# Optimization experiments

Measured on AMD Instinct MI355X. Metric: run time of the kernel, lower is better.

The kernel has to match this reference:

```python
import jax, jax.numpy as jnp
import numpy as np

N = 100000      # points
M = 12500       # cluster centers
E0 = 1600000    # point-level edges
E1 = 400000     # cluster-level edges
F_IN = 4        # raw point feature dim (e.g. intensity + extras)
D = 64          # hidden feature width
N_CLASSES = 8


def setup_inputs() -> dict:
    key = jax.random.key(0)
    ks = jax.random.split(key, 20)
    s = 0.05
    d = {}
    d["features"] = jax.random.normal(ks[0], (N, F_IN), jnp.float32)
    d["points"] = jax.random.normal(ks[1], (N, 3), jnp.float32)
    d["cluster_centers"] = jax.random.normal(ks[2], (M, 3), jnp.float32)
    d["l0_edges"] = jax.random.randint(ks[3], (E0, 2), 0, N)
    d["l1_edges"] = jax.random.randint(ks[4], (E1, 2), 0, M)
    d["labels"] = jax.random.randint(ks[5], (N,), 0, M)
    # Feature_extract MLP
    d["W_fe"] = s * jax.random.normal(ks[6], (F_IN + 3, D), jnp.float32)
    d["b_fe"] = jnp.zeros((D,), jnp.float32)
    # 4 Mini_GNN layers (layer2, layer2_1, layer6, layer6_1), stacked
    d["mini_We"] = s * jax.random.normal(ks[7], (4, D + 3, D), jnp.float32)
    d["mini_be"] = jnp.zeros((4, D), jnp.float32)
    d["mini_Wu"] = s * jax.random.normal(ks[8], (4, D, D), jnp.float32)
    d["mini_bu"] = jnp.zeros((4, D), jnp.float32)
    # Mini_to_Large
    d["W_m1"] = s * jax.random.normal(ks[9], (D + 3, D), jnp.float32)
    d["b_m1"] = jnp.zeros((D,), jnp.float32)
    d["W_m2"] = s * jax.random.normal(ks[10], (D, D), jnp.float32)
    d["b_m2"] = jnp.zeros((D,), jnp.float32)
    # 2 GNN layers on cluster graph (layer4, layer4_1), stacked
    d["gnn_We"] = s * jax.random.normal(ks[11], (2, D + 3, D), jnp.float32)
    d["gnn_be"] = jnp.zeros((2, D), jnp.float32)
    d["gnn_Wu"] = s * jax.random.normal(ks[12], (2, D, D), jnp.float32)
    d["gnn_bu"] = jnp.zeros((2, D), jnp.float32)
    # Large_to_Mini
    d["W_l"] = s * jax.random.normal(ks[13], (D + 3, D), jnp.float32)
    d["b_l"] = jnp.zeros((D,), jnp.float32)
    # Classifier
    d["W_c"] = s * jax.random.normal(ks[14], (D, N_CLASSES), jnp.float32)
    d["b_c"] = jnp.zeros((N_CLASSES,), jnp.float32)
    return d


def _gnn_layer(feat, pos, edges, We, be, Wu, bu, n_nodes):
    """PointGNN-style layer: gather -> edge MLP -> scatter max -> update MLP -> residual."""
    src, dst = edges[:, 0], edges[:, 1]
    e_in = jnp.concatenate([pos[src] - pos[dst], feat[src]], axis=-1)  # [E, 3+D]
    h = jax.nn.relu(e_in @ We + be)                                     # [E, D]
    agg = jax.ops.segment_max(h, dst, num_segments=n_nodes)            # [n, D]
    agg = jnp.where(jnp.isneginf(agg), 0.0, agg)  # nodes with no in-edges -> 0
    return jax.nn.relu(agg @ Wu + bu) + feat


def reference(features, points, cluster_centers, l0_edges, l1_edges, labels,
              W_fe, b_fe, mini_We, mini_be, mini_Wu, mini_bu,
              W_m1, b_m1, W_m2, b_m2, gnn_We, gnn_be, gnn_Wu, gnn_bu,
              W_l, b_l, W_c, b_c):
    rel = points - cluster_centers[labels]  # [N, 3] point pos relative to its cluster
    # layer1: Feature_extract
    f1 = jax.nn.relu(jnp.concatenate([features, rel], -1) @ W_fe + b_fe)
    # layer2 / layer2_1: Mini_GNN (scatter max) on point graph
    f2 = _gnn_layer(f1, points, l0_edges, mini_We[0], mini_be[0], mini_Wu[0], mini_bu[0], N)
    f2_1 = _gnn_layer(f2, points, l0_edges, mini_We[1], mini_be[1], mini_Wu[1], mini_bu[1], N)
    # layer3: Mini_to_Large (scatter sum by labels)
    h = jax.nn.relu(jnp.concatenate([f2_1, rel], -1) @ W_m1 + b_m1)
    c = jax.ops.segment_sum(h, labels, num_segments=M)  # [M, D]
    f3 = jax.nn.relu(c @ W_m2 + b_m2)
    # layer4 / layer4_1: GNN (scatter max) on cluster graph
    f4 = _gnn_layer(f3, cluster_centers, l1_edges, gnn_We[0], gnn_be[0], gnn_Wu[0], gnn_bu[0], M)
    f4_1 = _gnn_layer(f4, cluster_centers, l1_edges, gnn_We[1], gnn_be[1], gnn_Wu[1], gnn_bu[1], M)
    # layer5: Large_to_Mini (gather by labels)
    f5 = jax.nn.relu(jnp.concatenate([f4_1[labels], rel], -1) @ W_l + b_l)
    # layer6 / layer6_1 with residual skips per call()
    f6 = _gnn_layer(f5, points, l0_edges, mini_We[2], mini_be[2], mini_Wu[2], mini_bu[2], N)
    f6 = f6 + f2_1
    f6_1 = _gnn_layer(f6, points, l0_edges, mini_We[3], mini_be[3], mini_Wu[3], mini_bu[3], N)
    final = f6_1 + f2
    return final @ W_c + b_c  # [N, N_CLASSES] per-point logits
```

## Files before the change

### kernel.cpp

```cpp
#include <hip/hip_runtime.h>


#define N_PTS   100000
#define M_CL    12500
#define E0_N    1600000
#define E1_N    400000

#define NB      256
#define NCOPY   32
#define RANGE0  391
#define RANGE1  49
#define NCH0    782
#define NCH1    196
#define NCHL    49
#define CAP0    7168
#define CAP1    2048
#define CAPL    768

#define LSTR    72

typedef unsigned short ushortT;
typedef short  short8 __attribute__((ext_vector_type(8)));
typedef short  s4v    __attribute__((ext_vector_type(4)));
typedef float  v4f    __attribute__((ext_vector_type(4)));
typedef _Float16 h2   __attribute__((ext_vector_type(2)));
typedef unsigned u4v  __attribute__((ext_vector_type(4)));

__device__ inline ushortT f2bf(float x){
  union{float f; unsigned u;} v; v.f = x;
  unsigned r = v.u + 0x7fffu + ((v.u >> 16) & 1u);
  return (ushortT)(r >> 16);
}
__device__ inline float bf2f(ushortT h){
  union{unsigned u; float f;} v; v.u = ((unsigned)h) << 16;
  return v.f;
}
__device__ inline ushortT f2h(float x){
  union{_Float16 h; ushortT u;} v; v.h = (_Float16)x;
  return v.u;
}
__device__ inline float h2f(ushortT u){
  union{ushortT u; _Float16 h;} v; v.u = u;
  return (float)v.h;
}
__device__ inline h2 pkmax(h2 a, h2 b){ return __builtin_elementwise_max(a, b); }
__device__ inline h2 u2h(unsigned u){ union{unsigned u; h2 h;} v{u}; return v.h; }


struct WSrc { const float* p[22]; };

__global__ __launch_bounds__(256) void k_init_wprep(WSrc s, ushortT* __restrict__ wt, ushortT* __restrict__ wtc,
                                                    float* __restrict__ wpp,
                                                    int* b0, int* b1, int* bL){
  int blk = blockIdx.x;
  if (blk == 0){
    int t = threadIdx.x;
    #pragma unroll
    for (int k=0;k<NCOPY;++k){
      b0[k*NB + t] = 0; b1[k*NB + t] = 0; bL[k*NB + t] = 0;
    }
    return;
  }
  int slot = blk - 1;
  if (slot < 15){
    const float* src = s.p[slot];
    ushortT* dst = wt + slot*4096;
    for (int e=threadIdx.x; e<4096; e+=256){
      int nn = e>>6, p = e&63;
      int kk = (p&3)*16 + (p>>2);
      dst[e] = f2bf(src[kk*64+nn]);
    }
  } else if (slot == 15){
    const float* src = s.p[15];
    for (int e=threadIdx.x; e<1024; e+=256){
      int nn = e>>6, p = e&63;
      int kk = (p&3)*16 + (p>>2);
      wtc[e] = (nn<8) ? f2bf(src[kk*8+nn]) : (ushortT)0;
    }
  } else {
    for (int e=threadIdx.x; e<6*192; e+=256){
      int i = e/192, rem = e - i*192, r = rem>>6, p = rem&63;
      wpp[e] = s.p[16+i][r*64 + ((p&3)*16 + (p>>2))];
    }
  }
}


template<int RANGE, bool LAB>
__device__ void sort_chunk(const int* __restrict__ edges, int E, int c,
                           unsigned* __restrict__ slab, int* __restrict__ offC,
                           int* __restrict__ btot,
                           unsigned* slds, int* hist, int* pfx){
  int tid = threadIdx.x;
  int base = c*2048;
  int cnt = E - base; if (cnt > 2048) cnt = 2048;
  hist[tid] = 0;
  __syncthreads();
  int bk[8]; unsigned pk[8];
  #pragma unroll
  for (int r=0;r<8;++r){
    int e = base + r*256 + tid;
    bk[r] = -1; pk[r] = 0;
    if (e < E){
      int s, d;
      if (LAB){ s = e; d = edges[e]; }
      else    { int2 ed = ((const int2*)edges)[e]; s = ed.x; d = ed.y; }
      int b = d / RANGE;
      bk[r] = b;
      pk[r] = ((unsigned)s << 11) | (unsigned)(d - b*RANGE);
      atomicAdd(&hist[b], 1);
    }
  }
  __syncthreads();
  int own = hist[tid];
  pfx[tid] = own;
  __syncthreads();
  for (int st=1; st<256; st<<=1){
    int x = (tid >= st) ? pfx[tid-st] : 0;
    __syncthreads();
    pfx[tid] += x;
    __syncthreads();
  }
  int excl = pfx[tid] - own;
  offC[(size_t)c*257 + tid] = excl;
  if (tid == 0) offC[(size_t)c*257 + 256] = cnt;
  if (own) atomicAdd(&btot[(c & (NCOPY-1))*NB + tid], own);
  hist[tid] = excl;
  __syncthreads();
  #pragma unroll
  for (int r=0;r<8;++r){
    if (bk[r] >= 0){
      int pos = atomicAdd(&hist[bk[r]], 1);
      slds[pos] = pk[r];
    }
  }
  __syncthreads();
  unsigned* sg = slab + (size_t)c*2048;
  for (int i=tid; i<cnt; i+=256) sg[i] = slds[i];
}


template<int RANGE, int NCHUNK, int CAP, int K>
__device__ void csr_build_seg(const unsigned* __restrict__ slab, const int* __restrict__ offC,
                              const int* __restrict__ btot,
                              int n, int* __restrict__ offs, int* __restrict__ csr,
                              int b, unsigned* stage, int* hist, int* part){
  constexpr int CPT = (NCHUNK + 255) / 256;
  int tid = threadIdx.x;
  int dlo = b*RANGE;
  int range = n - dlo; if (range > RANGE) range = RANGE; if (range < 0) range = 0;
  int ownT = 0;
  #pragma unroll
  for (int k=0;k<NCOPY;++k) ownT += btot[k*NB + tid];
  part[tid] = ownT;
  __syncthreads();
  for (int st=1; st<256; st<<=1){
    int x = (tid >= st) ? part[tid-st] : 0;
    __syncthreads();
    part[tid] += x;
    __syncthreads();
  }
  int totB = part[b];
  int total = part[NB-1];
  if (b == NB-1 && tid == 0) offs[n] = total;
  __syncthreads();
  int mst[CPT], mlen[CPT];
  int csum = 0;
  #pragma unroll
  for (int k=0;k<CPT;++k){
    int c = tid + k*256;
    int l = 0, s0 = 0;
    if (c < NCHUNK){
      s0 = offC[(size_t)c*257 + b];
      l  = offC[(size_t)c*257 + b + 1] - s0;
    }
    mst[k] = s0; mlen[k] = l; csum += l;
  }
  part[tid] = csum;
  __syncthreads();
  int own2 = csum;
  for (int st=1; st<256; st<<=1){
    int x = (tid >= st) ? part[tid-st] : 0;
    __syncthreads();
    part[tid] += x;
    __syncthreads();
  }
  int cnt = part[NB-1];
  int gb = totB - cnt;
  int sb = part[tid] - own2;
  #pragma unroll
  for (int k=0;k<CPT;++k){
    int c = tid + k*256;
    if (c < NCHUNK){
      const unsigned* sg = slab + (size_t)c*2048 + mst[k];
      for (int j=0;j<mlen[k];++j) stage[sb+j] = sg[j];
      sb += mlen[k];
    }
  }
  __syncthreads();
  for (int t=tid; t<RANGE; t+=256) hist[t] = 0;
  __syncthreads();
  for (int j=tid; j<cnt; j+=256) atomicAdd(&hist[stage[j] & 2047u], 1);
  __syncthreads();
  int s = 0; int loc[K];
  #pragma unroll
  for (int kk=0; kk<K; ++kk){
    int idx = tid*K + kk;
    int v = (idx < RANGE) ? hist[idx] : 0;
    loc[kk] = s; s += v;
  }
  part[tid] = s; __syncthreads();
  int own3 = s;
  for (int st=1; st<256; st<<=1){
    int x = (tid >= st) ? part[tid-st] : 0;
    __syncthreads();
    part[tid] += x;
    __syncthreads();
  }
  int ebase = part[tid] - own3;
  __syncthreads();
  #pragma unroll
  for (int kk=0; kk<K; ++kk){
    int idx = tid*K + kk;
    if (idx < RANGE){
      int ex = ebase + loc[kk];
      if (idx < range) offs[dlo+idx] = gb + ex;
      hist[idx] = ex;
    }
  }
  __syncthreads();
  for (int j=tid; j<cnt; j+=256){
    unsigned p = stage[j];
    int pos = atomicAdd(&hist[p & 2047u], 1);
    csr[gb + pos] = (int)(p >> 11);
  }
}

__global__ __launch_bounds__(256) void k_build_all(
    const unsigned* s0, const int* oc0, const int* bt0, int* offs0, int* csr0,
    const unsigned* s1, const int* oc1, const int* bt1, int* offs1, int* csr1,
    const unsigned* sL, const int* ocL, const int* btL, int* offsL, int* csrL){
  __shared__ unsigned stage[CAP0];
  __shared__ int hist[RANGE0];
  __shared__ int part[256];
  int b = blockIdx.x;
  if (b < 256)      csr_build_seg<RANGE0,NCH0,CAP0,2>(s0, oc0, bt0, N_PTS, offs0, csr0, b, stage, hist, part);
  else if (b < 512) csr_build_seg<RANGE1,NCH1,CAP1,1>(s1, oc1, bt1, M_CL, offs1, csr1, b-256, stage, hist, part);
  else              csr_build_seg<RANGE1,NCHL,CAPL,1>(sL, ocL, btL, M_CL, offsL, csrL, b-512, stage, hist, part);
}


__global__ __launch_bounds__(256) void k_bin_f1g(
    const int* __restrict__ l0e, const int* __restrict__ l1e, const int* __restrict__ labels,
    int* bt0, int* bt1, int* btL,
    unsigned* s0, unsigned* s1, unsigned* sL,
    int* oc0, int* oc1, int* ocL,
    const float* __restrict__ features, const float* __restrict__ points,
    const float* __restrict__ centers,
    const float* __restrict__ W, const float* __restrict__ bfe,
    const ushortT* __restrict__ Wt2, const float* __restrict__ bias2,
    const float* __restrict__ Wr2,
    float* __restrict__ rel, ushortT* __restrict__ f1b,
    ushortT* __restrict__ gout, int n, int ntiles, int nf1blk)
{
  __shared__ char smem[10240];
  int b = blockIdx.x;
  if (b < 1027){
    unsigned* slds = (unsigned*)smem;
    int* hist = (int*)(smem + 8192);
    int* pfx  = (int*)(smem + 9216);
    if (b < 782)      sort_chunk<RANGE0,false>(l0e, E0_N, b,     s0, oc0, bt0, slds, hist, pfx);
    else if (b < 978) sort_chunk<RANGE1,false>(l1e, E1_N, b-782, s1, oc1, bt1, slds, hist, pfx);
    else              sort_chunk<RANGE1,true >(labels, N_PTS, b-978, sL, ocL, btL, slds, hist, pfx);
    return;
  }
  ushortT* lds = (ushortT*)smem;
  int bb = b - 1027;
  int tid = threadIdx.x;
  int lane = tid & 63, wslot = tid >> 6;
  int quad = lane >> 4, l15 = lane & 15;
  int permL = (lane & 15)*4 + (lane >> 4);
  int r3 = lane/3, c3 = lane - r3*3;
  int gw = (bb*256 + tid) >> 6;
  int nw = (nf1blk*256) >> 6;
  float Wf0=W[0*64+lane], Wf1=W[1*64+lane], Wf2=W[2*64+lane], Wf3=W[3*64+lane];
  float wr0=W[4*64+lane], wr1=W[5*64+lane], wr2=W[6*64+lane];
  float bias=bfe[lane];
  short8 s0_0 = *(const short8*)(Wt2 + ( 0 + l15)*64 +  0 + quad*8);
  short8 s0_1 = *(const short8*)(Wt2 + ( 0 + l15)*64 + 32 + quad*8);
  short8 s1_0 = *(const short8*)(Wt2 + (16 + l15)*64 +  0 + quad*8);
  short8 s1_1 = *(const short8*)(Wt2 + (16 + l15)*64 + 32 + quad*8);
  short8 s2_0 = *(const short8*)(Wt2 + (32 + l15)*64 +  0 + quad*8);
  short8 s2_1 = *(const short8*)(Wt2 + (32 + l15)*64 + 32 + quad*8);
  short8 s3_0 = *(const short8*)(Wt2 + (48 + l15)*64 +  0 + quad*8);
  short8 s3_1 = *(const short8*)(Wt2 + (48 + l15)*64 + 32 + quad*8);
  float eb0 = bias2[l15], eb1 = bias2[16+l15], eb2 = bias2[32+l15], eb3 = bias2[48+l15];
  float e0c0=Wr2[0*64+l15], e0c1=Wr2[0*64+16+l15], e0c2=Wr2[0*64+32+l15], e0c3=Wr2[0*64+48+l15];
  float e1c0=Wr2[1*64+l15], e1c1=Wr2[1*64+16+l15], e1c2=Wr2[1*64+32+l15], e1c3=Wr2[1*64+48+l15];
  float e2c0=Wr2[2*64+l15], e2c1=Wr2[2*64+16+l15], e2c2=Wr2[2*64+32+l15], e2c3=Wr2[2*64+48+l15];

  for (int t=gw; t<ntiles; t+=nw){
    int i0 = t*16;
    int lab16 = labels[min(i0 + (lane & 15), n-1)];
    float fv  = features[(size_t)min(i0 + (lane>>2), n-1)*4 + (lane & 3)];
    int lb = __shfl(lab16, (r3 < 16) ? r3 : 0, 64);
    float pv = 0.f, relv = 0.f;
    if (lane < 48){
      int rowp = i0 + r3;
      int rc = (rowp < n) ? rowp : (n-1);
      pv = points[(size_t)rc*3 + c3];
      float cv = centers[(size_t)lb*3 + c3];
      relv = pv - cv;
      if (rowp < n) rel[(size_t)rowp*3 + c3] = relv;
    }
    #pragma unroll
    for (int r=0;r<16;++r){
      float rx = __shfl(relv, 3*r+0, 64);
      float ry = __shfl(relv, 3*r+1, 64);
      float rz = __shfl(relv, 3*r+2, 64);
      float f0 = __shfl(fv, 4*r+0, 64);
      float f1 = __shfl(fv, 4*r+1, 64);
      float f2 = __shfl(fv, 4*r+2, 64);
      float f3 = __shfl(fv, 4*r+3, 64);
      float acc = bias + wr0*rx + wr1*ry + wr2*rz;
      acc += f0*Wf0 + f1*Wf1;
      acc += f2*Wf2 + f3*Wf3;
      acc = fmaxf(acc, 0.f);
      ushortT ab = f2bf(acc);
      int row = i0 + r;
      if (row < n) f1b[(size_t)row*64 + permL] = ab;
      lds[wslot*(16*LSTR) + r*LSTR + permL] = ab;
    }
    __builtin_amdgcn_wave_barrier();
    const ushortT* lp = lds + wslot*(16*LSTR) + l15*LSTR + quad*8;
    short8 sa0 = *(const short8*)(lp);
    short8 sa1 = *(const short8*)(lp + 32);
    __builtin_amdgcn_wave_barrier();
    v4f ec0 = {0.f,0.f,0.f,0.f}, ec1 = ec0, ec2 = ec0, ec3 = ec0;
    ec0 = __builtin_amdgcn_mfma_f32_16x16x32_bf16(sa0, s0_0, ec0, 0,0,0);
    ec1 = __builtin_amdgcn_mfma_f32_16x16x32_bf16(sa0, s1_0, ec1, 0,0,0);
    ec2 = __builtin_amdgcn_mfma_f32_16x16x32_bf16(sa0, s2_0, ec2, 0,0,0);
    ec3 = __builtin_amdgcn_mfma_f32_16x16x32_bf16(sa0, s3_0, ec3, 0,0,0);
    ec0 = __builtin_amdgcn_mfma_f32_16x16x32_bf16(sa1, s0_1, ec0, 0,0,0);
    ec1 = __builtin_amdgcn_mfma_f32_16x16x32_bf16(sa1, s1_1, ec1, 0,0,0);
    ec2 = __builtin_amdgcn_mfma_f32_16x16x32_bf16(sa1, s2_1, ec2, 0,0,0);
    ec3 = __builtin_amdgcn_mfma_f32_16x16x32_bf16(sa1, s3_1, ec3, 0,0,0);
    #pragma unroll
    for (int r=0;r<4;++r){
      int row = i0 + quad*4 + r;
      if (row < n){
        int rr4 = quad*4 + r;
        float vx = __shfl(pv, 3*rr4+0, 64);
        float vy = __shfl(pv, 3*rr4+1, 64);
        float vz = __shfl(pv, 3*rr4+2, 64);
        float g0 = ec0[r] + eb0 + vx*e0c0 + vy*e1c0 + vz*e2c0;
        float g1 = ec1[r] + eb1 + vx*e0c1 + vy*e1c1 + vz*e2c1;
        float g2 = ec2[r] + eb2 + vx*e0c2 + vy*e1c2 + vz*e2c2;
        float g3 = ec3[r] + eb3 + vx*e0c3 + vy*e1c3 + vz*e2c3;
        s4v o; o.x=(short)f2h(g0); o.y=(short)f2h(g1); o.z=(short)f2h(g2); o.w=(short)f2h(g3);
        *(s4v*)(gout + (size_t)row*64 + l15*4) = o;
      }
    }
  }
}


template<bool RELU, int NRES, bool USEREL, bool GATHER, bool OUT16, bool F16O, int EMODE, bool ERELU>
__global__ __launch_bounds__(256) void k_gemm(
    const ushortT* __restrict__ A, const ushortT* __restrict__ Wt,
    const float* __restrict__ bias, const float* __restrict__ Wr,
    const float* __restrict__ rel, const int* __restrict__ gidx,
    const ushortT* __restrict__ r1, const ushortT* __restrict__ r2,
    ushortT* __restrict__ out16,
    const ushortT* __restrict__ Wt2, const float* __restrict__ bias2,
    const float* __restrict__ Wr2, const float* __restrict__ vec2,
    void* __restrict__ eout,
    int n, int ntiles)
{
  constexpr int LDSZ = (EMODE>0) ? 4*16*LSTR : 4;
  __shared__ ushortT lds[LDSZ];
  int tid = threadIdx.x;
  int lane = tid & 63, wslot = tid >> 6;
  int quad = lane >> 4, l15 = lane & 15;
  int r3 = lane/3, c3 = lane - r3*3;
  int gw = (blockIdx.x*256 + tid) >> 6;
  int nw = (gridDim.x*256) >> 6;

  short8 bfr0_0 = *(const short8*)(Wt + ( 0 + l15)*64 +  0 + quad*8);
  short8 bfr0_1 = *(const short8*)(Wt + ( 0 + l15)*64 + 32 + quad*8);
  short8 bfr1_0 = *(const short8*)(Wt + (16 + l15)*64 +  0 + quad*8);
  short8 bfr1_1 = *(const short8*)(Wt + (16 + l15)*64 + 32 + quad*8);
  short8 bfr2_0 = *(const short8*)(Wt + (32 + l15)*64 +  0 + quad*8);
  short8 bfr2_1 = *(const short8*)(Wt + (32 + l15)*64 + 32 + quad*8);
  short8 bfr3_0 = *(const short8*)(Wt + (48 + l15)*64 +  0 + quad*8);
  short8 bfr3_1 = *(const short8*)(Wt + (48 + l15)*64 + 32 + quad*8);
  float bs0 = bias[ 0 + l15], bs1 = bias[16 + l15];
  float bs2 = bias[32 + l15], bs3 = bias[48 + l15];
  float w0c0=0,w0c1=0,w0c2=0,w0c3=0, w1c0=0,w1c1=0,w1c2=0,w1c3=0, w2c0=0,w2c1=0,w2c2=0,w2c3=0;
  if (USEREL){
    w0c0=Wr[0*64+l15]; w0c1=Wr[0*64+16+l15]; w0c2=Wr[0*64+32+l15]; w0c3=Wr[0*64+48+l15];
    w1c0=Wr[1*64+l15]; w1c1=Wr[1*64+16+l15]; w1c2=Wr[1*64+32+l15]; w1c3=Wr[1*64+48+l15];
    w2c0=Wr[2*64+l15]; w2c1=Wr[2*64+16+l15]; w2c2=Wr[2*64+32+l15]; w2c3=Wr[2*64+48+l15];
  }

  short8 s0_0{}, s0_1{}, s1_0{}, s1_1{}, s2_0{}, s2_1{}, s3_0{}, s3_1{};
  float eb0=0, eb1=0, eb2=0, eb3=0;
  float e0c0=0,e0c1=0,e0c2=0,e0c3=0, e1c0=0,e1c1=0,e1c2=0,e1c3=0, e2c0=0,e2c1=0,e2c2=0,e2c3=0;
  float ebias_c = 0.f;
  if (EMODE == 1){
    s0_0 = *(const short8*)(Wt2 + ( 0 + l15)*64 +  0 + quad*8);
    s0_1 = *(const short8*)(Wt2 + ( 0 + l15)*64 + 32 + quad*8);
    s1_0 = *(const short8*)(Wt2 + (16 + l15)*64 +  0 + quad*8);
    s1_1 = *(const short8*)(Wt2 + (16 + l15)*64 + 32 + quad*8);
    s2_0 = *(const short8*)(Wt2 + (32 + l15)*64 +  0 + quad*8);
    s2_1 = *(const short8*)(Wt2 + (32 + l15)*64 + 32 + quad*8);
    s3_0 = *(const short8*)(Wt2 + (48 + l15)*64 +  0 + quad*8);
    s3_1 = *(const short8*)(Wt2 + (48 + l15)*64 + 32 + quad*8);
    eb0 = bias2[l15]; eb1 = bias2[16+l15]; eb2 = bias2[32+l15]; eb3 = bias2[48+l15];
    e0c0=Wr2[0*64+l15]; e0c1=Wr2[0*64+16+l15]; e0c2=Wr2[0*64+32+l15]; e0c3=Wr2[0*64+48+l15];
    e1c0=Wr2[1*64+l15]; e1c1=Wr2[1*64+16+l15]; e1c2=Wr2[1*64+32+l15]; e1c3=Wr2[1*64+48+l15];
    e2c0=Wr2[2*64+l15]; e2c1=Wr2[2*64+16+l15]; e2c2=Wr2[2*64+32+l15]; e2c3=Wr2[2*64+48+l15];
  } else if (EMODE == 2){
    s0_0 = *(const short8*)(Wt2 + l15*64 +  0 + quad*8);
    s0_1 = *(const short8*)(Wt2 + l15*64 + 32 + quad*8);
    ebias_c = (l15 < 8) ? bias2[l15] : 0.f;
  }

  for (int t=gw; t<ntiles; t+=nw){
    int i0 = t*16;
    int rowA = i0 + l15; if (rowA >= n) rowA = n-1;
    if (GATHER) rowA = gidx[rowA];
    const ushortT* ap = A + (size_t)rowA*64 + quad*8;
    short8 a0 = *(const short8*)(ap);
    short8 a1 = *(const short8*)(ap + 32);
    float relL = 0.f;
    if (USEREL && lane < 48){
      int rc = i0 + r3; if (rc >= n) rc = n-1;
      relL = rel[(size_t)rc*3 + c3];
    }
    v4f ac0 = {0.f,0.f,0.f,0.f}, ac1 = ac0, ac2 = ac0, ac3 = ac0;
    ac0 = __builtin_amdgcn_mfma_f32_16x16x32_bf16(a0, bfr0_0, ac0, 0,0,0);
    ac1 = __builtin_amdgcn_mfma_f32_16x16x32_bf16(a0, bfr1_0, ac1, 0,0,0);
    ac2 = __builtin_amdgcn_mfma_f32_16x16x32_bf16(a0, bfr2_0, ac2, 0,0,0);
    ac3 = __builtin_amdgcn_mfma_f32_16x16x32_bf16(a0, bfr3_0, ac3, 0,0,0);
    ac0 = __builtin_amdgcn_mfma_f32_16x16x32_bf16(a1, bfr0_1, ac0, 0,0,0);
    ac1 = __builtin_amdgcn_mfma_f32_16x16x32_bf16(a1, bfr1_1, ac1, 0,0,0);
    ac2 = __builtin_amdgcn_mfma_f32_16x16x32_bf16(a1, bfr2_1, ac2, 0,0,0);
    ac3 = __builtin_amdgcn_mfma_f32_16x16x32_bf16(a1, bfr3_1, ac3, 0,0,0);

    #pragma unroll
    for (int r=0;r<4;++r){
      int row = i0 + quad*4 + r;
      bool rowok = (row < n);
      float v0 = ac0[r] + bs0, v1 = ac1[r] + bs1, v2 = ac2[r] + bs2, v3 = ac3[r] + bs3;
      if (USEREL){
        int rr4 = quad*4 + r;
        float rx = __shfl(relL, 3*rr4+0, 64);
        float ry = __shfl(relL, 3*rr4+1, 64);
        float rz = __shfl(relL, 3*rr4+2, 64);
        v0 += rx*w0c0 + ry*w1c0 + rz*w2c0;
        v1 += rx*w0c1 + ry*w1c1 + rz*w2c1;
        v2 += rx*w0c2 + ry*w1c2 + rz*w2c2;
        v3 += rx*w0c3 + ry*w1c3 + rz*w2c3;
      }
      if (RELU){ v0=fmaxf(v0,0.f); v1=fmaxf(v1,0.f); v2=fmaxf(v2,0.f); v3=fmaxf(v3,0.f); }
      size_t pb = (size_t)row*64 + l15*4;
      if (rowok){
        if (NRES>=1){
          s4v rv = *(const s4v*)(r1 + pb);
          v0 += bf2f((ushortT)rv.x); v1 += bf2f((ushortT)rv.y);
          v2 += bf2f((ushortT)rv.z); v3 += bf2f((ushortT)rv.w);
        }
        if (NRES>=2){
          s4v rv = *(const s4v*)(r2 + pb);
          v0 += bf2f((ushortT)rv.x); v1 += bf2f((ushortT)rv.y);
          v2 += bf2f((ushortT)rv.z); v3 += bf2f((ushortT)rv.w);
        }
        if (OUT16){
          s4v o;
          if (F16O){ o.x=(short)f2h(v0); o.y=(short)f2h(v1); o.z=(short)f2h(v2); o.w=(short)f2h(v3); }
          else     { o.x=(short)f2bf(v0); o.y=(short)f2bf(v1); o.z=(short)f2bf(v2); o.w=(short)f2bf(v3); }
          *(s4v*)(out16 + pb) = o;
        }
      }
      if (EMODE > 0){
        int lb = wslot*(16*LSTR) + (quad*4+r)*LSTR + l15*4;
        s4v o; o.x=(short)f2bf(v0); o.y=(short)f2bf(v1); o.z=(short)f2bf(v2); o.w=(short)f2bf(v3);
        *(s4v*)(lds + lb) = o;
      }
    }

    if (EMODE > 0){
      __builtin_amdgcn_wave_barrier();
      const ushortT* lp = lds + wslot*(16*LSTR) + l15*LSTR + quad*8;
      short8 sa0 = *(const short8*)(lp);
      short8 sa1 = *(const short8*)(lp + 32);
      __builtin_amdgcn_wave_barrier();
      if (EMODE == 1){
        float posv = 0.f;
        if (lane < 48){
          int rc = i0 + r3; if (rc >= n) rc = n-1;
          posv = vec2[(size_t)rc*3 + c3];
        }
        v4f ec0 = {0.f,0.f,0.f,0.f}, ec1 = ec0, ec2 = ec0, ec3 = ec0;
        ec0 = __builtin_amdgcn_mfma_f32_16x16x32_bf16(sa0, s0_0, ec0, 0,0,0);
        ec1 = __builtin_amdgcn_mfma_f32_16x16x32_bf16(sa0, s1_0, ec1, 0,0,0);
        ec2 = __builtin_amdgcn_mfma_f32_16x16x32_bf16(sa0, s2_0, ec2, 0,0,0);
        ec3 = __builtin_amdgcn_mfma_f32_16x16x32_bf16(sa0, s3_0, ec3, 0,0,0);
        ec0 = __builtin_amdgcn_mfma_f32_16x16x32_bf16(sa1, s0_1, ec0, 0,0,0);
        ec1 = __builtin_amdgcn_mfma_f32_16x16x32_bf16(sa1, s1_1, ec1, 0,0,0);
        ec2 = __builtin_amdgcn_mfma_f32_16x16x32_bf16(sa1, s2_1, ec2, 0,0,0);
        ec3 = __builtin_amdgcn_mfma_f32_16x16x32_bf16(sa1, s3_1, ec3, 0,0,0);
        ushortT* eo = (ushortT*)eout;
        #pragma unroll
        for (int r=0;r<4;++r){
          int row = i0 + quad*4 + r;
          if (row < n){
            int rr4 = quad*4 + r;
            float vx = __shfl(posv, 3*rr4+0, 64);
            float vy = __shfl(posv, 3*rr4+1, 64);
            float vz = __shfl(posv, 3*rr4+2, 64);
            float g0 = ec0[r] + eb0 + vx*e0c0 + vy*e1c0 + vz*e2c0;
            float g1 = ec1[r] + eb1 + vx*e0c1 + vy*e1c1 + vz*e2c1;
            float g2 = ec2[r] + eb2 + vx*e0c2 + vy*e1c2 + vz*e2c2;
            float g3 = ec3[r] + eb3 + vx*e0c3 + vy*e1c3 + vz*e2c3;
            if (ERELU){ g0=fmaxf(g0,0.f); g1=fmaxf(g1,0.f); g2=fmaxf(g2,0.f); g3=fmaxf(g3,0.f); }
            s4v o; o.x=(short)f2h(g0); o.y=(short)f2h(g1); o.z=(short)f2h(g2); o.w=(short)f2h(g3);
            *(s4v*)(eo + (size_t)row*64 + l15*4) = o;
          }
        }
      } else {
        v4f ec = {0.f,0.f,0.f,0.f};
        ec = __builtin_amdgcn_mfma_f32_16x16x32_bf16(sa0, s0_0, ec, 0,0,0);
        ec = __builtin_amdgcn_mfma_f32_16x16x32_bf16(sa1, s0_1, ec, 0,0,0);
        if (l15 < 8){
          float* eo = (float*)eout;
          #pragma unroll
          for (int r=0;r<4;++r){
            int row = i0 + quad*4 + r;
            if (row < n) eo[(size_t)row*8 + l15] = ec[r] + ebias_c;
          }
        }
      }
    }
  }
}


__global__ __launch_bounds__(256) void k_edge_agg(const int* __restrict__ offs, const int* __restrict__ csr,
                                                  const float* __restrict__ pos, const ushortT* __restrict__ g,
                                                  const float* __restrict__ Wp, ushortT* __restrict__ agg, int n){
  int lane = threadIdx.x & 63;
  int grp = lane >> 3, d8 = lane & 7;
  int gbase = lane & 56;
  int gw = (blockIdx.x*256 + threadIdx.x) >> 6;
  int nw = (gridDim.x*256) >> 6;
  const u4v* g4 = (const u4v*)g;
  float2 w0[4], w1[4], w2[4];
  #pragma unroll
  for (int q=0;q<4;++q){
    w0[q] = *(const float2*)(Wp + 0*64 + d8*8 + 2*q);
    w1[q] = *(const float2*)(Wp + 1*64 + d8*8 + 2*q);
    w2[q] = *(const float2*)(Wp + 2*64 + d8*8 + 2*q);
  }
  const h2 NEGBIG = {(_Float16)-60000.f, (_Float16)-60000.f};
  int n8 = (n+7) >> 3;
  for (int ii=gw; ii<n8; ii+=nw){
    int i0 = ii*8;
    int ig = i0 + grp; bool ok = ig < n; if (!ok) ig = n-1;
    int b = offs[ig], e = offs[ig+1];
    int cnt = e - b, c1 = cnt - 1;
    int mx = cnt;
    mx = max(mx, __shfl_xor(mx, 8, 64));
    mx = max(mx, __shfl_xor(mx, 16, 64));
    mx = max(mx, __shfl_xor(mx, 32, 64));
    h2 m0=NEGBIG, m1=NEGBIG, m2=NEGBIG, m3=NEGBIG;
    for (int J=0; J<mx; J+=8){
      if (J < cnt){
        int sv = csr[b + min(J + d8, c1)];
        #pragma unroll
        for (int jj=0; jj<8; ++jj){
          int s = __shfl(sv, gbase + jj, 64);
          u4v u = g4[(size_t)s*8 + d8];
          m0 = pkmax(m0, u2h(u.x));
          m1 = pkmax(m1, u2h(u.y));
          m2 = pkmax(m2, u2h(u.z));
          m3 = pkmax(m3, u2h(u.w));
        }
      }
    }
    float px = pos[ig*3+0], py = pos[ig*3+1], pz = pos[ig*3+2];
    u4v outv;
    {
      float sA = w0[0].x*px + w1[0].x*py + w2[0].x*pz;
      float sB = w0[0].y*px + w1[0].y*py + w2[0].y*pz;
      outv.x = (unsigned)f2bf(fmaxf((float)m0.x - sA, 0.f)) |
               ((unsigned)f2bf(fmaxf((float)m0.y - sB, 0.f)) << 16);
    }
    {
      float sA = w0[1].x*px + w1[1].x*py + w2[1].x*pz;
      float sB = w0[1].y*px + w1[1].y*py + w2[1].y*pz;
      outv.y = (unsigned)f2bf(fmaxf((float)m1.x - sA, 0.f)) |
               ((unsigned)f2bf(fmaxf((float)m1.y - sB, 0.f)) << 16);
    }
    {
      float sA = w0[2].x*px + w1[2].x*py + w2[2].x*pz;
      float sB = w0[2].y*px + w1[2].y*py + w2[2].y*pz;
      outv.z = (unsigned)f2bf(fmaxf((float)m2.x - sA, 0.f)) |
               ((unsigned)f2bf(fmaxf((float)m2.y - sB, 0.f)) << 16);
    }
    {
      float sA = w0[3].x*px + w1[3].x*py + w2[3].x*pz;
      float sB = w0[3].y*px + w1[3].y*py + w2[3].y*pz;
      outv.w = (unsigned)f2bf(fmaxf((float)m3.x - sA, 0.f)) |
               ((unsigned)f2bf(fmaxf((float)m3.y - sB, 0.f)) << 16);
    }
    if (ok) ((u4v*)agg)[(size_t)ig*8 + d8] = outv;
  }
}


__global__ __launch_bounds__(256) void k_seg_gather(const int* __restrict__ offs, const int* __restrict__ csr,
                                                    const ushortT* __restrict__ h, ushortT* __restrict__ c, int m){
  int lane = threadIdx.x & 63;
  int wv = (blockIdx.x*256 + threadIdx.x) >> 6;
  if (wv >= m) return;
  int b = offs[wv], e = offs[wv+1];
  float acc = 0.f;
  for (int k=b; k<e; ++k){
    int i = csr[k];
    acc += h2f(h[(size_t)i*64+lane]);
  }
  c[(size_t)wv*64+lane] = f2bf(acc);
}


extern "C" void kernel_launch(void* const* d_in, const int* in_sizes, int n_in,
                              void* d_out, int out_size, void* d_ws, size_t ws_size,
                              hipStream_t stream){
  const float* features = (const float*)d_in[0];
  const float* points   = (const float*)d_in[1];
  const float* centers  = (const float*)d_in[2];
  const int*   l0e      = (const int*)d_in[3];
  const int*   l1e      = (const int*)d_in[4];
  const int*   labels   = (const int*)d_in[5];
  const float* W_fe = (const float*)d_in[6];
  const float* b_fe = (const float*)d_in[7];
  const float* mWe  = (const float*)d_in[8];
  const float* mbe  = (const float*)d_in[9];
  const float* mWu  = (const float*)d_in[10];
  const float* mbu  = (const float*)d_in[11];
  const float* W_m1 = (const float*)d_in[12];
  const float* b_m1 = (const float*)d_in[13];
  const float* W_m2 = (const float*)d_in[14];
  const float* b_m2 = (const float*)d_in[15];
  const float* gWe  = (const float*)d_in[16];
  const float* gbe  = (const float*)d_in[17];
  const float* gWu  = (const float*)d_in[18];
  const float* gbu  = (const float*)d_in[19];
  const float* W_l  = (const float*)d_in[20];
  const float* b_l  = (const float*)d_in[21];
  const float* W_c  = (const float*)d_in[22];
  const float* b_c  = (const float*)d_in[23];
  float* out = (float*)d_out;

  char* w = (char*)d_ws;
  size_t off = 0;
  auto alloc = [&](size_t bytes)->void*{
    void* p = (void*)(w + off);
    off = (off + bytes + 255) & ~(size_t)255;
    return p;
  };
  float* rel  = (float*)alloc((size_t)N_PTS*3*4);
  ushortT* UF1 = (ushortT*)alloc((size_t)N_PTS*64*2);
  ushortT* UF2 = (ushortT*)alloc((size_t)N_PTS*64*2);
  ushortT* UF21= (ushortT*)alloc((size_t)N_PTS*64*2);
  ushortT* UF5 = (ushortT*)alloc((size_t)N_PTS*64*2);
  ushortT* UF6 = (ushortT*)alloc((size_t)N_PTS*64*2);
  ushortT* gbuf= (ushortT*)alloc((size_t)N_PTS*64*2);
  ushortT* abuf= (ushortT*)alloc((size_t)N_PTS*64*2);
  ushortT* cb_b= (ushortT*)alloc((size_t)M_CL*64*2);
  ushortT* UF3 = (ushortT*)alloc((size_t)M_CL*64*2);
  ushortT* UF4 = (ushortT*)alloc((size_t)M_CL*64*2);
  ushortT* cg_b= (ushortT*)alloc((size_t)M_CL*64*2);
  ushortT* cagg_b = (ushortT*)alloc((size_t)M_CL*64*2);
  ushortT* f41_b  = (ushortT*)alloc((size_t)M_CL*64*2);
  ushortT* wt  = (ushortT*)alloc((size_t)15*4096*2);
  ushortT* wtc = (ushortT*)alloc((size_t)1024*2);
  float* wpp = (float*)alloc((size_t)6*192*4);
  int* offs0 = (int*)alloc((size_t)(N_PTS+1)*4);
  int* csr0  = (int*)alloc((size_t)E0_N*4);
  int* offs1 = (int*)alloc((size_t)(M_CL+1)*4);
  int* csr1  = (int*)alloc((size_t)E1_N*4);
  int* offsL = (int*)alloc((size_t)(M_CL+1)*4);
  int* csrL  = (int*)alloc((size_t)N_PTS*4);
  unsigned* slab0 = (unsigned*)alloc((size_t)NCH0*2048*4);
  unsigned* slab1 = (unsigned*)alloc((size_t)NCH1*2048*4);
  unsigned* slabL = (unsigned*)alloc((size_t)NCHL*2048*4);
  int* offC0 = (int*)alloc((size_t)NCH0*257*4);
  int* offC1 = (int*)alloc((size_t)NCH1*257*4);
  int* offCL = (int*)alloc((size_t)NCHL*257*4);
  int* btot0 = (int*)alloc((size_t)NCOPY*NB*4);
  int* btot1 = (int*)alloc((size_t)NCOPY*NB*4);
  int* btotL = (int*)alloc((size_t)NCOPY*NB*4);
  (void)ws_size; (void)in_sizes; (void)n_in; (void)out_size;

  const int NT_N = (N_PTS+15)/16;
  const int NT_M = (M_CL +15)/16;
  const int GBG_N = 1563;
  const int GBG_M = 196;
  const int GB_N  = 3125;
  const int GB_BIN = 1027;

  WSrc ws{};
  ws.p[0]=mWu+0*4096; ws.p[1]=mWu+1*4096; ws.p[2]=mWu+2*4096; ws.p[3]=mWu+3*4096;
  ws.p[4]=W_m2; ws.p[5]=gWu+0*4096; ws.p[6]=gWu+1*4096;
  ws.p[7]=mWe+0*4288+192; ws.p[8]=mWe+1*4288+192; ws.p[9]=mWe+2*4288+192; ws.p[10]=mWe+3*4288+192;
  ws.p[11]=W_m1; ws.p[12]=W_l; ws.p[13]=gWe+0*4288+192; ws.p[14]=gWe+1*4288+192;
  ws.p[15]=W_c;
  ws.p[16]=mWe+0*4288; ws.p[17]=mWe+1*4288; ws.p[18]=mWe+2*4288; ws.p[19]=mWe+3*4288;
  ws.p[20]=gWe+0*4288; ws.p[21]=gWe+1*4288;
  k_init_wprep<<<18, 256, 0, stream>>>(ws, wt, wtc, wpp, btot0, btot1, btotL);
  k_bin_f1g<<<GB_BIN + GBG_N, 256, 0, stream>>>(l0e, l1e, labels, btot0, btot1, btotL,
      slab0, slab1, slabL, offC0, offC1, offCL,
      features, points, centers, W_fe, b_fe,
      wt+7*4096, mbe+0, mWe+0*4288, rel, UF1, gbuf, N_PTS, NT_N, GBG_N);
  k_build_all<<<768, 256, 0, stream>>>(slab0, offC0, btot0, offs0, csr0,
                                       slab1, offC1, btot1, offs1, csr1,
                                       slabL, offCL, btotL, offsL, csrL);

  k_edge_agg<<<GB_N,256,0,stream>>>(offs0, csr0, points, gbuf, wpp+0*192, abuf, N_PTS);
  k_gemm<true,1,false,false,true,false,1,false><<<GBG_N,256,0,stream>>>(abuf, wt+0*4096, mbu+0,
      nullptr, nullptr, nullptr, UF1, nullptr, UF2,
      wt+8*4096, mbe+64, mWe+1*4288, points, gbuf, N_PTS, NT_N);
  k_edge_agg<<<GB_N,256,0,stream>>>(offs0, csr0, points, gbuf, wpp+1*192, abuf, N_PTS);
  k_gemm<true,1,false,false,true,false,1,true><<<GBG_N,256,0,stream>>>(abuf, wt+1*4096, mbu+64,
      nullptr, nullptr, nullptr, UF2, nullptr, UF21,
      wt+11*4096, b_m1, W_m1+4096, rel, gbuf, N_PTS, NT_N);
  k_seg_gather<<<(M_CL*64+255)/256, 256, 0, stream>>>(offsL, csrL, gbuf, cb_b, M_CL);
  k_gemm<true,0,false,false,true,false,1,false><<<GBG_M,256,0,stream>>>(cb_b, wt+4*4096, b_m2,
      nullptr, nullptr, nullptr, nullptr, nullptr, UF3,
      wt+13*4096, gbe+0, gWe+0*4288, centers, cg_b, M_CL, NT_M);
  k_edge_agg<<<GBG_M,256,0,stream>>>(offs1, csr1, centers, cg_b, wpp+4*192, cagg_b, M_CL);
  k_gemm<true,1,false,false,true,false,1,false><<<GBG_M,256,0,stream>>>(cagg_b, wt+5*4096, gbu+0,
      nullptr, nullptr, nullptr, UF3, nullptr, UF4,
      wt+14*4096, gbe+64, gWe+1*4288, centers, cg_b, M_CL, NT_M);
  k_edge_agg<<<GBG_M,256,0,stream>>>(offs1, csr1, centers, cg_b, wpp+5*192, cagg_b, M_CL);
  k_gemm<true,1,false,false,true,false,0,false><<<GBG_M,256,0,stream>>>(cagg_b, wt+6*4096, gbu+64,
      nullptr, nullptr, nullptr, UF4, nullptr, f41_b,
      nullptr, nullptr, nullptr, nullptr, nullptr, M_CL, NT_M);
  k_gemm<true,0,true,true,true,false,1,false><<<GBG_N,256,0,stream>>>(f41_b, wt+12*4096, b_l,
      W_l+4096, rel, labels, nullptr, nullptr, UF5,
      wt+9*4096, mbe+128, mWe+2*4288, points, gbuf, N_PTS, NT_N);
  k_edge_agg<<<GB_N,256,0,stream>>>(offs0, csr0, points, gbuf, wpp+2*192, abuf, N_PTS);
  k_gemm<true,2,false,false,true,false,1,false><<<GBG_N,256,0,stream>>>(abuf, wt+2*4096, mbu+128,
      nullptr, nullptr, nullptr, UF5, UF21, UF6,
      wt+10*4096, mbe+192, mWe+3*4288, points, gbuf, N_PTS, NT_N);
  k_edge_agg<<<GB_N,256,0,stream>>>(offs0, csr0, points, gbuf, wpp+3*192, abuf, N_PTS);
  k_gemm<true,2,false,false,false,false,2,false><<<GBG_N,256,0,stream>>>(abuf, wt+3*4096, mbu+192,
      nullptr, nullptr, nullptr, UF6, UF2, nullptr,
      wtc, b_c, nullptr, nullptr, out, N_PTS, NT_N);
}
```

Measured before the change: 459.6 us.

## Fold weight prep into binning kernel and parallelize CSR slab copy

```diff
diff --git a/kernel.cpp b/kernel.cpp
--- a/kernel.cpp
+++ b/kernel.cpp
@@ -46,44 +46,7 @@
 __device__ inline h2 pkmax(h2 a, h2 b){ return __builtin_elementwise_max(a, b); }
 __device__ inline h2 u2h(unsigned u){ union{unsigned u; h2 h;} v{u}; return v.h; }
 
-
 struct WSrc { const float* p[22]; };
-
-__global__ __launch_bounds__(256) void k_init_wprep(WSrc s, ushortT* __restrict__ wt, ushortT* __restrict__ wtc,
-                                                    float* __restrict__ wpp,
-                                                    int* b0, int* b1, int* bL){
-  int blk = blockIdx.x;
-  if (blk == 0){
-    int t = threadIdx.x;
-    #pragma unroll
-    for (int k=0;k<NCOPY;++k){
-      b0[k*NB + t] = 0; b1[k*NB + t] = 0; bL[k*NB + t] = 0;
-    }
-    return;
-  }
-  int slot = blk - 1;
-  if (slot < 15){
-    const float* src = s.p[slot];
-    ushortT* dst = wt + slot*4096;
-    for (int e=threadIdx.x; e<4096; e+=256){
-      int nn = e>>6, p = e&63;
-      int kk = (p&3)*16 + (p>>2);
-      dst[e] = f2bf(src[kk*64+nn]);
-    }
-  } else if (slot == 15){
-    const float* src = s.p[15];
-    for (int e=threadIdx.x; e<1024; e+=256){
-      int nn = e>>6, p = e&63;
-      int kk = (p&3)*16 + (p>>2);
-      wtc[e] = (nn<8) ? f2bf(src[kk*8+nn]) : (ushortT)0;
-    }
-  } else {
-    for (int e=threadIdx.x; e<6*192; e+=256){
-      int i = e/192, rem = e - i*192, r = rem>>6, p = rem&63;
-      wpp[e] = s.p[16+i][r*64 + ((p&3)*16 + (p>>2))];
-    }
-  }
-}
 
 
 template<int RANGE, bool LAB>
@@ -140,11 +103,12 @@
 }
 
 
-template<int RANGE, int NCHUNK, int CAP, int K>
+template<int RANGE, int NCHUNK, int K>
 __device__ void csr_build_seg(const unsigned* __restrict__ slab, const int* __restrict__ offC,
                               const int* __restrict__ btot,
                               int n, int* __restrict__ offs, int* __restrict__ csr,
-                              int b, unsigned* stage, int* hist, int* part){
+                              int b, unsigned* stage, int* hist, int* part,
+                              ushortT* mstA, ushortT* mlenA, ushortT* sbA){
   constexpr int CPT = (NCHUNK + 255) / 256;
   int tid = threadIdx.x;
   int dlo = b*RANGE;
@@ -192,9 +156,29 @@
   for (int k=0;k<CPT;++k){
     int c = tid + k*256;
     if (c < NCHUNK){
-      const unsigned* sg = slab + (size_t)c*2048 + mst[k];
-      for (int j=0;j<mlen[k];++j) stage[sb+j] = sg[j];
+      mstA[c] = (ushortT)mst[k];
+      mlenA[c] = (ushortT)mlen[k];
+      sbA[c] = (ushortT)sb;
       sb += mlen[k];
+    }
+  }
+  __syncthreads();
+  int wv = tid >> 6, l = tid & 63;
+  for (int cb = wv*32; cb < NCHUNK; cb += 128){
+    int c = cb + (l >> 1);
+    if (c < NCHUNK){
+      int len = mlenA[c];
+      int half = l & 1;
+      if (half*4 < len){
+        const unsigned* sg = slab + (size_t)c*2048 + mstA[c];
+        int sbc = sbA[c];
+        for (int j = half*4; j < len; j += 8){
+          unsigned v[4];
+          __builtin_memcpy(v, sg + j, 16);
+          #pragma unroll
+          for (int q=0;q<4;++q) if (j+q < len) stage[sbc+j+q] = v[q];
+        }
+      }
     }
   }
   __syncthreads();
@@ -243,35 +227,64 @@
   __shared__ unsigned stage[CAP0];
   __shared__ int hist[RANGE0];
   __shared__ int part[256];
+  __shared__ ushortT mstA[NCH0];
+  __shared__ ushortT mlenA[NCH0];
+  __shared__ ushortT sbA[NCH0];
   int b = blockIdx.x;
-  if (b < 256)      csr_build_seg<RANGE0,NCH0,CAP0,2>(s0, oc0, bt0, N_PTS, offs0, csr0, b, stage, hist, part);
-  else if (b < 512) csr_build_seg<RANGE1,NCH1,CAP1,1>(s1, oc1, bt1, M_CL, offs1, csr1, b-256, stage, hist, part);
-  else              csr_build_seg<RANGE1,NCHL,CAPL,1>(sL, ocL, btL, M_CL, offsL, csrL, b-512, stage, hist, part);
+  if (b < 256)      csr_build_seg<RANGE0,NCH0,2>(s0, oc0, bt0, N_PTS, offs0, csr0, b, stage, hist, part, mstA, mlenA, sbA);
+  else if (b < 512) csr_build_seg<RANGE1,NCH1,1>(s1, oc1, bt1, M_CL, offs1, csr1, b-256, stage, hist, part, mstA, mlenA, sbA);
+  else              csr_build_seg<RANGE1,NCHL,1>(sL, ocL, btL, M_CL, offsL, csrL, b-512, stage, hist, part, mstA, mlenA, sbA);
 }
 
 
 __global__ __launch_bounds__(256) void k_bin_f1g(
+    WSrc s, ushortT* __restrict__ wt, ushortT* __restrict__ wtc, float* __restrict__ wpp,
     const int* __restrict__ l0e, const int* __restrict__ l1e, const int* __restrict__ labels,
     int* bt0, int* bt1, int* btL,
-    unsigned* s0, unsigned* s1, unsigned* sL,
+    unsigned* sl0, unsigned* sl1, unsigned* slL,
     int* oc0, int* oc1, int* ocL,
     const float* __restrict__ features, const float* __restrict__ points,
     const float* __restrict__ centers,
     const float* __restrict__ W, const float* __restrict__ bfe,
-    const ushortT* __restrict__ Wt2, const float* __restrict__ bias2,
-    const float* __restrict__ Wr2,
+    const float* __restrict__ bias2, const float* __restrict__ We,
     float* __restrict__ rel, ushortT* __restrict__ f1b,
     ushortT* __restrict__ gout, int n, int ntiles, int nf1blk)
 {
   __shared__ char smem[10240];
   int b = blockIdx.x;
+  if (b < 17){
+    int slot = b;
+    if (slot < 15){
+      const float* src = s.p[slot];
+      ushortT* dst = wt + slot*4096;
+      for (int e=threadIdx.x; e<4096; e+=256){
+        int nn = e>>6, p = e&63;
+        int kk = (p&3)*16 + (p>>2);
+        dst[e] = f2bf(src[kk*64+nn]);
+      }
+    } else if (slot == 15){
+      const float* src = s.p[15];
+      for (int e=threadIdx.x; e<1024; e+=256){
+        int nn = e>>6, p = e&63;
+        int kk = (p&3)*16 + (p>>2);
+        wtc[e] = (nn<8) ? f2bf(src[kk*8+nn]) : (ushortT)0;
+      }
+    } else {
+      for (int e=threadIdx.x; e<6*192; e+=256){
+        int i = e/192, rem = e - i*192, r = rem>>6, p = rem&63;
+        wpp[e] = s.p[16+i][r*64 + ((p&3)*16 + (p>>2))];
+      }
+    }
+    return;
+  }
+  b -= 17;
   if (b < 1027){
     unsigned* slds = (unsigned*)smem;
     int* hist = (int*)(smem + 8192);
     int* pfx  = (int*)(smem + 9216);
-    if (b < 782)      sort_chunk<RANGE0,false>(l0e, E0_N, b,     s0, oc0, bt0, slds, hist, pfx);
-    else if (b < 978) sort_chunk<RANGE1,false>(l1e, E1_N, b-782, s1, oc1, bt1, slds, hist, pfx);
-    else              sort_chunk<RANGE1,true >(labels, N_PTS, b-978, sL, ocL, btL, slds, hist, pfx);
+    if (b < 782)      sort_chunk<RANGE0,false>(l0e, E0_N, b,     sl0, oc0, bt0, slds, hist, pfx);
+    else if (b < 978) sort_chunk<RANGE1,false>(l1e, E1_N, b-782, sl1, oc1, bt1, slds, hist, pfx);
+    else              sort_chunk<RANGE1,true >(labels, N_PTS, b-978, slL, ocL, btL, slds, hist, pfx);
     return;
   }
   ushortT* lds = (ushortT*)smem;
@@ -286,18 +299,25 @@
   float Wf0=W[0*64+lane], Wf1=W[1*64+lane], Wf2=W[2*64+lane], Wf3=W[3*64+lane];
   float wr0=W[4*64+lane], wr1=W[5*64+lane], wr2=W[6*64+lane];
   float bias=bfe[lane];
-  short8 s0_0 = *(const short8*)(Wt2 + ( 0 + l15)*64 +  0 + quad*8);
-  short8 s0_1 = *(const short8*)(Wt2 + ( 0 + l15)*64 + 32 + quad*8);
-  short8 s1_0 = *(const short8*)(Wt2 + (16 + l15)*64 +  0 + quad*8);
-  short8 s1_1 = *(const short8*)(Wt2 + (16 + l15)*64 + 32 + quad*8);
-  short8 s2_0 = *(const short8*)(Wt2 + (32 + l15)*64 +  0 + quad*8);
-  short8 s2_1 = *(const short8*)(Wt2 + (32 + l15)*64 + 32 + quad*8);
-  short8 s3_0 = *(const short8*)(Wt2 + (48 + l15)*64 +  0 + quad*8);
-  short8 s3_1 = *(const short8*)(Wt2 + (48 + l15)*64 + 32 + quad*8);
+  const float* Wk = We + 192;
+  auto ldf = [&](int nn, int pbase)->short8{
+    short8 r;
+    #pragma unroll
+    for (int e=0;e<8;++e){
+      int p = pbase + e;
+      int kk = (p&3)*16 + (p>>2);
+      r[e] = (short)f2bf(Wk[kk*64 + nn]);
+    }
+    return r;
+  };
+  short8 s0_0 = ldf(l15, quad*8),      s0_1 = ldf(l15, 32+quad*8);
+  short8 s1_0 = ldf(16+l15, quad*8),   s1_1 = ldf(16+l15, 32+quad*8);
+  short8 s2_0 = ldf(32+l15, quad*8),   s2_1 = ldf(32+l15, 32+quad*8);
+  short8 s3_0 = ldf(48+l15, quad*8),   s3_1 = ldf(48+l15, 32+quad*8);
   float eb0 = bias2[l15], eb1 = bias2[16+l15], eb2 = bias2[32+l15], eb3 = bias2[48+l15];
-  float e0c0=Wr2[0*64+l15], e0c1=Wr2[0*64+16+l15], e0c2=Wr2[0*64+32+l15], e0c3=Wr2[0*64+48+l15];
-  float e1c0=Wr2[1*64+l15], e1c1=Wr2[1*64+16+l15], e1c2=Wr2[1*64+32+l15], e1c3=Wr2[1*64+48+l15];
-  float e2c0=Wr2[2*64+l15], e2c1=Wr2[2*64+16+l15], e2c2=Wr2[2*64+32+l15], e2c3=Wr2[2*64+48+l15];
+  float e0c0=We[0*64+l15], e0c1=We[0*64+16+l15], e0c2=We[0*64+32+l15], e0c3=We[0*64+48+l15];
+  float e1c0=We[1*64+l15], e1c1=We[1*64+16+l15], e1c2=We[1*64+32+l15], e1c3=We[1*64+48+l15];
+  float e2c0=We[2*64+l15], e2c1=We[2*64+16+l15], e2c2=We[2*64+32+l15], e2c3=We[2*64+48+l15];
 
   for (int t=gw; t<ntiles; t+=nw){
     int i0 = t*16;
@@ -700,9 +720,10 @@
   int* offC0 = (int*)alloc((size_t)NCH0*257*4);
   int* offC1 = (int*)alloc((size_t)NCH1*257*4);
   int* offCL = (int*)alloc((size_t)NCHL*257*4);
-  int* btot0 = (int*)alloc((size_t)NCOPY*NB*4);
-  int* btot1 = (int*)alloc((size_t)NCOPY*NB*4);
-  int* btotL = (int*)alloc((size_t)NCOPY*NB*4);
+  int* btotA = (int*)alloc((size_t)3*NCOPY*NB*4);
+  int* btot0 = btotA;
+  int* btot1 = btotA + NCOPY*NB;
+  int* btotL = btotA + 2*NCOPY*NB;
   (void)ws_size; (void)in_sizes; (void)n_in; (void)out_size;
 
   const int NT_N = (N_PTS+15)/16;
@@ -710,7 +731,7 @@
   const int GBG_N = 1563;
   const int GBG_M = 196;
   const int GB_N  = 3125;
-  const int GB_BIN = 1027;
+  const int GB_BIN = 17 + 1027;
 
   WSrc ws{};
   ws.p[0]=mWu+0*4096; ws.p[1]=mWu+1*4096; ws.p[2]=mWu+2*4096; ws.p[3]=mWu+3*4096;
@@ -720,11 +741,13 @@
   ws.p[15]=W_c;
   ws.p[16]=mWe+0*4288; ws.p[17]=mWe+1*4288; ws.p[18]=mWe+2*4288; ws.p[19]=mWe+3*4288;
   ws.p[20]=gWe+0*4288; ws.p[21]=gWe+1*4288;
-  k_init_wprep<<<18, 256, 0, stream>>>(ws, wt, wtc, wpp, btot0, btot1, btotL);
-  k_bin_f1g<<<GB_BIN + GBG_N, 256, 0, stream>>>(l0e, l1e, labels, btot0, btot1, btotL,
+
+  hipMemsetAsync(btotA, 0, (size_t)3*NCOPY*NB*4, stream);
+  k_bin_f1g<<<GB_BIN + GBG_N, 256, 0, stream>>>(ws, wt, wtc, wpp,
+      l0e, l1e, labels, btot0, btot1, btotL,
       slab0, slab1, slabL, offC0, offC1, offCL,
-      features, points, centers, W_fe, b_fe,
-      wt+7*4096, mbe+0, mWe+0*4288, rel, UF1, gbuf, N_PTS, NT_N, GBG_N);
+      features, points, centers, W_fe, b_fe, mbe, mWe,
+      rel, UF1, gbuf, N_PTS, NT_N, GBG_N);
   k_build_all<<<768, 256, 0, stream>>>(slab0, offC0, btot0, offs0, csr0,
                                        slab1, offC1, btot1, offs1, csr1,
                                        slabL, offCL, btotL, offsL, csrL);
```

Measured after the change: 450.1 us (median of 2 runs). 1.02x faster.
